# Kernel tuning notes

Measured on AMD Instinct MI355X. Metric: run time of the kernel, lower is better.

Reference implementation:

```python
import jax, jax.numpy as jnp
import numpy as np

B, C, N, OUT, K = 8, 64, 4096, 64, 16


def setup_inputs() -> dict:
    key = jax.random.key(0)
    k0, k1, k2, k3, k4 = jax.random.split(key, 5)
    x = jax.random.normal(k0, (B, C, N, 1), jnp.float32)
    s1 = 1.0 / np.sqrt(2 * C)
    s2 = 1.0 / np.sqrt(OUT)
    W1 = jax.random.uniform(k1, (2 * C, OUT), jnp.float32, -s1, s1)
    b1 = jax.random.uniform(k2, (OUT,), jnp.float32, -s1, s1)
    W2 = jax.random.uniform(k3, (OUT, OUT), jnp.float32, -s2, s2)
    b2 = jax.random.uniform(k4, (OUT,), jnp.float32, -s2, s2)
    return {"x": x, "W1": W1, "b1": b1, "W2": W2, "b2": b2}


def reference(x, W1, b1, W2, b2):
    # x: [B, C, N, 1] -> node features [B, N, C]
    xb = x[..., 0].transpose(0, 2, 1)  # [B, N, C]
    # kNN per batch element (PyG knn includes the point itself)
    sq = jnp.sum(xb * xb, axis=-1)  # [B, N]
    d2 = sq[:, :, None] + sq[:, None, :] - 2.0 * jnp.einsum('bnc,bmc->bnm', xb, xb)
    _, idx = jax.lax.top_k(-d2, K)  # [B, N, K] neighbor indices
    # gather neighbor features: [B, N, K, C]
    xj = jax.vmap(lambda f, i: jnp.take(f, i, axis=0))(xb, idx)
    xi = xb[:, :, None, :]  # [B, N, 1, C]
    # EdgeConv edge features: [x_i, x_j - x_i]
    e = jnp.concatenate([jnp.broadcast_to(xi, xj.shape), xj - xi], axis=-1)  # [B,N,K,2C]
    h = jax.nn.relu(e @ W1 + b1)
    h = jax.nn.relu(h @ W2 + b2)
    out = jnp.max(h, axis=2)  # max aggregation over neighbors -> [B, N, OUT]
    return out.transpose(0, 2, 1)[..., None]  # [B, OUT, N, 1]
```

## Files before the change

### kernel.cpp

```cpp
#include <hip/hip_runtime.h>
#include <stdint.h>

#define BB 8
#define CCH 64
#define NPB 4096
#define NPTS (BB*NPB)
#define PPW 8

typedef float  f32x2  __attribute__((ext_vector_type(2)));
typedef float  f32x4v __attribute__((ext_vector_type(4)));
typedef short  bf16x8 __attribute__((ext_vector_type(8)));
typedef unsigned short u16x8 __attribute__((ext_vector_type(8)));
typedef unsigned long long u64;
typedef unsigned int u32;

__device__ __forceinline__ unsigned short f2bf(float x) {
    u32 u = __float_as_uint(x);
    u += 0x7FFFu + ((u >> 16) & 1u);
    return (unsigned short)(u >> 16);
}

template<typename T>
__device__ __forceinline__ void sort16(T* key) {
#pragma unroll
    for (int kk = 2; kk <= 16; kk <<= 1) {
#pragma unroll
        for (int j = kk >> 1; j > 0; j >>= 1) {
#pragma unroll
            for (int i = 0; i < 16; ++i) {
                int l = i ^ j;
                if (l > i) {
                    bool up = ((i & kk) == 0);
                    T a = key[i], c = key[l];
                    bool cond = up ? (c < a) : (a < c);
                    key[i] = cond ? c : a;
                    key[l] = cond ? a : c;
                }
            }
        }
    }
}

template<typename T>
__device__ __forceinline__ void merge16(T* list, const T* key) {
    T m[16];
#pragma unroll
    for (int i = 0; i < 16; ++i) {
        T a = list[i], c = key[15 - i];
        m[i] = (c < a) ? c : a;
    }
#pragma unroll
    for (int j = 8; j > 0; j >>= 1) {
#pragma unroll
        for (int i = 0; i < 16; ++i) {
            if ((i & j) == 0) {
                T a = m[i], c = m[i + j];
                bool cond = c < a;
                m[i]     = cond ? c : a;
                m[i + j] = cond ? a : c;
            }
        }
    }
#pragma unroll
    for (int i = 0; i < 16; ++i) list[i] = m[i];
}

__global__ void k_transpose(const float* __restrict__ x, float* __restrict__ xb,
                            unsigned short* __restrict__ xh, float* __restrict__ sq) {
    __shared__ float tile[64][65];
    int b  = blockIdx.y;
    int n0 = blockIdx.x * 64;
    int tx = threadIdx.x, ty = threadIdx.y;
    const float* xp = x + (size_t)b * CCH * NPB;
#pragma unroll
    for (int r = 0; r < 8; ++r) {
        int c = ty + r * 8;
        tile[c][tx] = xp[(size_t)c * NPB + n0 + tx];
    }
    __syncthreads();
    float* xbp = xb + ((size_t)b * NPB + n0) * CCH;
    unsigned short* xhp = xh + ((size_t)b * NPB + n0) * CCH;
    float* sqp = sq + (size_t)b * NPB + n0;
#pragma unroll
    for (int r = 0; r < 8; ++r) {
        int nn = ty + r * 8;
        float v = tile[tx][nn];
        xbp[(size_t)nn * CCH + tx] = v;
        xhp[(size_t)nn * CCH + tx] = f2bf(v);
        float s = v * v;
#pragma unroll
        for (int o = 32; o > 0; o >>= 1) s += __shfl_xor(s, o);
        if (tx == 0) sqp[nn] = s;
    }
}

__global__ void k_prepw(const float* __restrict__ W1, const float* __restrict__ W2,
                        unsigned short* __restrict__ W1t, unsigned short* __restrict__ W2t) {
    int t = blockIdx.x * 256 + threadIdx.x;
    if (t < 8192) {
        int o = t >> 7, k = t & 127;
        float v = (k < 64) ? (W1[k * 64 + o] - W1[(64 + k) * 64 + o]) : W1[k * 64 + o];
        W1t[o * 128 + k] = f2bf(v);
    } else if (t < 12288) {
        int u = t - 8192;
        int o = u >> 6, j = u & 63;
        W2t[o * 64 + j] = f2bf(W2[j * 64 + o]);
    }
}

__global__ __launch_bounds__(256) void k_gemm(const unsigned short* __restrict__ xh,
                                              const float* __restrict__ sq,
                                              u32* __restrict__ cand) {
    __shared__ float dtile[64][65];
    __shared__ u32 llist[64][65];
    int b = blockIdx.y >> 6;
    const unsigned short* xhB = xh + (size_t)b * NPB * CCH;
    const float* sqB = sq + (size_t)b * NPB;
    u32* candB = cand + (size_t)b * 64 * NPB * 16;
    int l = threadIdx.x & 63;
    int w = threadIdx.x >> 6;
    int m0 = (blockIdx.y & 63) * 64;
    int n0 = blockIdx.x * 64;
    const unsigned short* ap = xhB + (size_t)(m0 + w * 16 + (l & 15)) * CCH + ((l >> 4) * 8);
    bf16x8 a0 = *(const bf16x8*)ap;
    bf16x8 a1 = *(const bf16x8*)(ap + 32);
    f32x4v z = {0.f, 0.f, 0.f, 0.f};
    f32x4v acc[4];
#pragma unroll
    for (int cg = 0; cg < 4; ++cg) {
        const unsigned short* bp = xhB + (size_t)(n0 + cg * 16 + (l & 15)) * CCH + ((l >> 4) * 8);
        bf16x8 b0 = *(const bf16x8*)bp;
        bf16x8 b1 = *(const bf16x8*)(bp + 32);
        acc[cg] = __builtin_amdgcn_mfma_f32_16x16x32_bf16(a0, b0, z, 0, 0, 0);
        acc[cg] = __builtin_amdgcn_mfma_f32_16x16x32_bf16(a1, b1, acc[cg], 0, 0, 0);
    }
    int rb = m0 + w * 16 + (l >> 4) * 4;
    float4 sr = *(const float4*)(sqB + rb);
    float sqr[4] = {sr.x, sr.y, sr.z, sr.w};
#pragma unroll
    for (int cg = 0; cg < 4; ++cg) {
        int cit = cg * 16 + (l & 15);
        float sc = sqB[n0 + cit];
#pragma unroll
        for (int j = 0; j < 4; ++j) {
            float v = fmaxf(fmaf(-2.f, acc[cg][j], sqr[j] + sc), 0.f);
            dtile[w * 16 + (l >> 4) * 4 + j][cit] = v;
        }
    }
    __syncthreads();
    {
        int row = l, ch = w;
        u32 key[16];
#pragma unroll
        for (int e = 0; e < 16; ++e) {
            float v = dtile[row][ch * 16 + e];
            key[e] = ((u32)f2bf(v) << 16) | (u32)(n0 + ch * 16 + e);
        }
        sort16(key);
#pragma unroll
        for (int i = 0; i < 16; ++i) llist[row][ch * 16 + i] = key[i];
    }
    __syncthreads();
    if (threadIdx.x < 128) {
        int r2 = threadIdx.x & 63;
        int hf = threadIdx.x >> 6;
        u32 a[16], c[16];
#pragma unroll
        for (int i = 0; i < 16; ++i) a[i] = llist[r2][hf * 32 + i];
#pragma unroll
        for (int i = 0; i < 16; ++i) c[i] = llist[r2][hf * 32 + 16 + i];
        merge16(a, c);
#pragma unroll
        for (int i = 0; i < 16; ++i) llist[r2][hf * 32 + i] = a[i];
    }
    __syncthreads();
    if (threadIdx.x < 64) {
        int r2 = threadIdx.x;
        u32 list[16], tmp[16];
#pragma unroll
        for (int i = 0; i < 16; ++i) list[i] = llist[r2][i];
#pragma unroll
        for (int i = 0; i < 16; ++i) tmp[i] = llist[r2][32 + i];
        merge16(list, tmp);
        u32* cp = candB + ((size_t)blockIdx.x * NPB + (m0 + r2)) * 16;
#pragma unroll
        for (int i = 0; i < 16; ++i) cp[i] = list[i];
    }
}

__global__ __launch_bounds__(256, 1) void k_post(const u32* __restrict__ cand,
                                                 const float* __restrict__ xb,
                                                 const float* __restrict__ sq,
                                                 int* __restrict__ idxo) {
    __shared__ u32 slots[4][64];
    int l  = threadIdx.x & 63;
    int rl = __builtin_amdgcn_readfirstlane(threadIdx.x >> 6);
    int rowg = blockIdx.x * 4 + rl;
    int b    = rowg >> 12;
    int row  = rowg & 4095;
    const float* xbB = xb + ((size_t)b << 12) * CCH;
    const float* sqB = sq + ((size_t)b << 12);
    const u32* candB = cand + (size_t)b * 64 * NPB * 16;
    const float* xr = xbB + (size_t)row * CCH;
    float rr[64];
#pragma unroll
    for (int i = 0; i < 16; ++i) {
        float4 v = *(const float4*)(xr + i * 4);
        rr[4*i] = v.x; rr[4*i+1] = v.y; rr[4*i+2] = v.z; rr[4*i+3] = v.w;
    }
    u32 karr[16];
    {
        const uint4* cp = (const uint4*)(candB + ((size_t)l * NPB + row) * 16);
#pragma unroll
        for (int i = 0; i < 4; ++i) {
            uint4 v = cp[i];
            karr[4*i] = v.x; karr[4*i+1] = v.y; karr[4*i+2] = v.z; karr[4*i+3] = v.w;
        }
    }
    u32 lo = 0, hi = 0x7FFFu;
#pragma unroll
    for (int it = 0; it < 15; ++it) {
        u32 mid = (lo + hi) >> 1;
        int c = 0;
#pragma unroll
        for (int i = 0; i < 16; ++i) c += ((karr[i] >> 16) <= mid) ? 1 : 0;
#pragma unroll
        for (int o = 32; o > 0; o >>= 1) c += __shfl_xor(c, o);
        bool ge = (c >= 48);
        lo = ge ? lo : (mid + 1);
        hi = ge ? mid : hi;
    }
    u32 vstar = hi;
    int cnt = 0;
#pragma unroll
    for (int i = 0; i < 16; ++i) cnt += ((karr[i] >> 16) <= vstar) ? 1 : 0;
    int pre = cnt;
#pragma unroll
    for (int d = 1; d < 64; d <<= 1) {
        int t = __shfl_up(pre, d);
        if (l >= d) pre += t;
    }
    int base = pre - cnt;
    u32* sl = slots[rl];
    sl[l] = 0xFFFFFFFFu;
#pragma unroll
    for (int i = 0; i < 16; ++i) {
        if (i < cnt) {
            int s = base + i;
            if (s < 64) sl[s] = karr[i];
        }
    }
    u32 mk = sl[l];
    u64 key = ~0ULL;
    if (mk != 0xFFFFFFFFu) {
        int col = (int)(mk & 0xFFFFu);
        const float* xj = xbB + (size_t)col * CCH;
        float lod = 0.f, hid = 0.f;
#pragma unroll
        for (int q = 0; q < 8; ++q) {
            float4 v  = *(const float4*)(xj + q * 4);
            float4 wv = *(const float4*)(xj + 32 + q * 4);
            lod = fmaf(v.x,  rr[4*q+0], lod);
            lod = fmaf(v.y,  rr[4*q+1], lod);
            lod = fmaf(v.z,  rr[4*q+2], lod);
            lod = fmaf(v.w,  rr[4*q+3], lod);
            hid = fmaf(wv.x, rr[32+4*q+0], hid);
            hid = fmaf(wv.y, rr[32+4*q+1], hid);
            hid = fmaf(wv.z, rr[32+4*q+2], hid);
            hid = fmaf(wv.w, rr[32+4*q+3], hid);
        }
        float d = fmaf(-2.f, lod + hid, sqB[col]);
        u32 fb = __float_as_uint(d);
        fb ^= (fb >> 31) ? 0xFFFFFFFFu : 0x80000000u;
        key = ((u64)fb << 32) | (u32)col;
    }
#pragma unroll
    for (int kk = 2; kk <= 64; kk <<= 1) {
#pragma unroll
        for (int j = kk >> 1; j > 0; j >>= 1) {
            u64 p = (u64)__shfl_xor((long long)key, j);
            bool keep_min = (((l & kk) == 0) == ((l & j) == 0));
            bool plt = p < key;
            key = keep_min ? (plt ? p : key) : (plt ? key : p);
        }
    }
    if (l < 16) idxo[(size_t)rowg * 16 + l] = (int)(key & 0xFFFFFFFFu);
}

__global__ __launch_bounds__(256, 1) void k_mlp2(const unsigned short* __restrict__ xh,
                                                 const int* __restrict__ idx,
                                                 const unsigned short* __restrict__ W1t,
                                                 const unsigned short* __restrict__ W2t,
                                                 const float* __restrict__ b1,
                                                 const float* __restrict__ b2,
                                                 float* __restrict__ out) {
    __shared__ unsigned short h1l[4][16 * 72];
    int l   = threadIdx.x & 63;
    int wib = threadIdx.x >> 6;
    int e   = l & 15;
    int kg  = l >> 4;
    int wave = blockIdx.x * 4 + wib;
    unsigned short* hl = h1l[wib];

    bf16x8 w1f[4][4];
#pragma unroll
    for (int nt = 0; nt < 4; ++nt)
#pragma unroll
        for (int s = 0; s < 4; ++s)
            w1f[nt][s] = *(const bf16x8*)(W1t + (size_t)(nt * 16 + e) * 128 + s * 32 + kg * 8);
    bf16x8 w2f[4][2];
#pragma unroll
    for (int nt = 0; nt < 4; ++nt)
#pragma unroll
        for (int s = 0; s < 2; ++s)
            w2f[nt][s] = *(const bf16x8*)(W2t + (size_t)(nt * 16 + e) * 64 + s * 32 + kg * 8);
    float b1v[4], b2v[4];
#pragma unroll
    for (int nt = 0; nt < 4; ++nt) { b1v[nt] = b1[nt * 16 + e]; b2v[nt] = b2[nt * 16 + e]; }

    int p0 = wave * PPW;
    int bb = p0 >> 12;
    int n0 = p0 & 4095;
    const unsigned short* xhB = xh + ((size_t)bb << 12) * CCH;
    f32x4v z = {0.f, 0.f, 0.f, 0.f};
    float mx[4][PPW];
#pragma unroll
    for (int nt = 0; nt < 4; ++nt)
#pragma unroll
        for (int pi = 0; pi < PPW; ++pi) mx[nt][pi] = 0.f;

#pragma unroll
    for (int pi = 0; pi < PPW; ++pi) {
        int n = n0 + pi;
        int je = idx[((size_t)(p0 + pi)) * 16 + e];
        bf16x8 a[4];
        a[0] = *(const bf16x8*)(xhB + (size_t)n * 64 + kg * 8);
        a[1] = *(const bf16x8*)(xhB + (size_t)n * 64 + 32 + kg * 8);
        a[2] = *(const bf16x8*)(xhB + (size_t)je * 64 + kg * 8);
        a[3] = *(const bf16x8*)(xhB + (size_t)je * 64 + 32 + kg * 8);
#pragma unroll
        for (int nt = 0; nt < 4; ++nt) {
            f32x4v acc = z;
#pragma unroll
            for (int s = 0; s < 4; ++s)
                acc = __builtin_amdgcn_mfma_f32_16x16x32_bf16(a[s], w1f[nt][s], acc, 0, 0, 0);
#pragma unroll
            for (int j = 0; j < 4; ++j) {
                float h = fmaxf(acc[j] + b1v[nt], 0.f);
                hl[(kg * 4 + j) * 72 + nt * 16 + e] = f2bf(h);
            }
        }
        bf16x8 a2[2];
        a2[0] = *(const bf16x8*)(hl + (size_t)e * 72 + kg * 8);
        a2[1] = *(const bf16x8*)(hl + (size_t)e * 72 + 32 + kg * 8);
#pragma unroll
        for (int nt = 0; nt < 4; ++nt) {
            f32x4v acc = z;
            acc = __builtin_amdgcn_mfma_f32_16x16x32_bf16(a2[0], w2f[nt][0], acc, 0, 0, 0);
            acc = __builtin_amdgcn_mfma_f32_16x16x32_bf16(a2[1], w2f[nt][1], acc, 0, 0, 0);
            float m4 = 0.f;
#pragma unroll
            for (int j = 0; j < 4; ++j)
                m4 = fmaxf(m4, fmaxf(acc[j] + b2v[nt], 0.f));
            mx[nt][pi] = m4;
        }
    }
#pragma unroll
    for (int nt = 0; nt < 4; ++nt)
#pragma unroll
        for (int pi = 0; pi < PPW; ++pi) {
            float v = mx[nt][pi];
            v = fmaxf(v, __shfl_xor(v, 16));
            v = fmaxf(v, __shfl_xor(v, 32));
            mx[nt][pi] = v;
        }
    if (kg == 0) {
#pragma unroll
        for (int nt = 0; nt < 4; ++nt) {
            float* op = out + ((size_t)bb * 64 + nt * 16 + e) * NPB + n0;
#pragma unroll
            for (int pi = 0; pi < PPW; ++pi) op[pi] = mx[nt][pi];
        }
    }
}

extern "C" void kernel_launch(void* const* d_in, const int* in_sizes, int n_in,
                              void* d_out, int out_size, void* d_ws, size_t ws_size,
                              hipStream_t stream) {
    const float* x  = (const float*)d_in[0];
    const float* W1 = (const float*)d_in[1];
    const float* b1 = (const float*)d_in[2];
    const float* W2 = (const float*)d_in[3];
    const float* b2 = (const float*)d_in[4];
    float* out = (float*)d_out;

    const size_t MB = 1024 * 1024;
    char* ws = (char*)d_ws;
    float*          xb  = (float*)(ws);
    unsigned short* xh  = (unsigned short*)(ws + 8 * MB);
    float*          sq  = (float*)(ws + 12 * MB);
    unsigned short* W1t = (unsigned short*)(ws + 12 * MB + 256 * 1024);
    unsigned short* W2t = (unsigned short*)(ws + 12 * MB + 272 * 1024);
    u32*            cand = (u32*)(ws + 13 * MB);
    size_t candAll = (size_t)BB * 64 * NPB * 16 * 4;
    size_t needF = 13 * MB + candAll + (size_t)NPTS * 16 * 4;

    hipLaunchKernelGGL(k_transpose, dim3(NPB / 64, BB), dim3(64, 8), 0, stream, x, xb, xh, sq);
    hipLaunchKernelGGL(k_prepw, dim3(48), dim3(256), 0, stream, W1, W2, W1t, W2t);

    if (ws_size >= needF + MB) {
        int* idxb = (int*)(ws + 13 * MB + candAll);
        hipLaunchKernelGGL(k_gemm, dim3(NPB / 64, 64 * BB), dim3(256), 0, stream,
                           xh, sq, cand);
        hipLaunchKernelGGL(k_post, dim3(NPTS / 4), dim3(256), 0, stream,
                           cand, xb, sq, idxb);
        hipLaunchKernelGGL(k_mlp2, dim3(NPTS / PPW / 4), dim3(256), 0, stream,
                           xh, idxb, W1t, W2t, b1, b2, out);
    } else {
        int* idxb = (int*)(ws + 30 * MB);
        for (int b = 0; b < BB; ++b) {
            const unsigned short* xhB = xh + (size_t)b * NPB * CCH;
            const float* xbB = xb + (size_t)b * NPB * CCH;
            const float* sqB = sq + (size_t)b * NPB;
            hipLaunchKernelGGL(k_gemm, dim3(NPB / 64, 64), dim3(256), 0, stream,
                               xhB, sqB, cand);
            hipLaunchKernelGGL(k_post, dim3(NPB / 4), dim3(256), 0, stream,
                               cand, xbB, sqB, idxb + (size_t)b * NPB * 16);
        }
        hipLaunchKernelGGL(k_mlp2, dim3(NPTS / PPW / 4), dim3(256), 0, stream,
                           xh, idxb, W1t, W2t, b1, b2, out);
    }
}
```

Measured before the change: 321.5 us.

## Replace full candidate sort with sampled threshold, filtered rescan, and survivor rerank

A first pass sorts distances over a strided sample of 1024 columns per row (16 tiles of 64, n0 = blockIdx.x*256), and k_tau picks a bf16 distance threshold at the 16th-smallest of that sample. A second GEMM pass recomputes all distances and uses atomics to append columns at or under the threshold to a capped survivor list. k_sel then reranks the survivors exactly in fp32 with wave bitonic sorts. The aim is to drop the 64-way per-tile sort and the large candidate buffer write and read. The cost is a second GEMM pass, atomic contention, and possible truncation when more than 192 columns survive, which could lose true neighbours.

```diff
diff --git a/kernel.cpp b/kernel.cpp
--- a/kernel.cpp
+++ b/kernel.cpp
@@ -6,6 +6,7 @@
 #define NPB 4096
 #define NPTS (BB*NPB)
 #define PPW 8
+#define SCAP 192
 
 typedef float  f32x2  __attribute__((ext_vector_type(2)));
 typedef float  f32x4v __attribute__((ext_vector_type(4)));
@@ -108,15 +109,130 @@
     }
 }
 
-__global__ __launch_bounds__(256) void k_gemm(const unsigned short* __restrict__ xh,
-                                              const float* __restrict__ sq,
-                                              u32* __restrict__ cand) {
+__global__ __launch_bounds__(256) void k_gemm1(const unsigned short* __restrict__ xh,
+                                               const float* __restrict__ sq,
+                                               u32* __restrict__ cand16) {
     __shared__ float dtile[64][65];
     __shared__ u32 llist[64][65];
     int b = blockIdx.y >> 6;
     const unsigned short* xhB = xh + (size_t)b * NPB * CCH;
     const float* sqB = sq + (size_t)b * NPB;
-    u32* candB = cand + (size_t)b * 64 * NPB * 16;
+    u32* candB = cand16 + (size_t)b * 16 * NPB * 16;
+    int l = threadIdx.x & 63;
+    int w = threadIdx.x >> 6;
+    int m0 = (blockIdx.y & 63) * 64;
+    int n0 = blockIdx.x * 256;
+    const unsigned short* ap = xhB + (size_t)(m0 + w * 16 + (l & 15)) * CCH + ((l >> 4) * 8);
+    bf16x8 a0 = *(const bf16x8*)ap;
+    bf16x8 a1 = *(const bf16x8*)(ap + 32);
+    f32x4v z = {0.f, 0.f, 0.f, 0.f};
+    f32x4v acc[4];
+#pragma unroll
+    for (int cg = 0; cg < 4; ++cg) {
+        const unsigned short* bp = xhB + (size_t)(n0 + cg * 16 + (l & 15)) * CCH + ((l >> 4) * 8);
+        bf16x8 b0 = *(const bf16x8*)bp;
+        bf16x8 b1 = *(const bf16x8*)(bp + 32);
+        acc[cg] = __builtin_amdgcn_mfma_f32_16x16x32_bf16(a0, b0, z, 0, 0, 0);
+        acc[cg] = __builtin_amdgcn_mfma_f32_16x16x32_bf16(a1, b1, acc[cg], 0, 0, 0);
+    }
+    int rb = m0 + w * 16 + (l >> 4) * 4;
+    float4 sr = *(const float4*)(sqB + rb);
+    float sqr[4] = {sr.x, sr.y, sr.z, sr.w};
+#pragma unroll
+    for (int cg = 0; cg < 4; ++cg) {
+        int cit = cg * 16 + (l & 15);
+        float sc = sqB[n0 + cit];
+#pragma unroll
+        for (int j = 0; j < 4; ++j) {
+            float v = fmaxf(fmaf(-2.f, acc[cg][j], sqr[j] + sc), 0.f);
+            dtile[w * 16 + (l >> 4) * 4 + j][cit] = v;
+        }
+    }
+    __syncthreads();
+    {
+        int row = l, ch = w;
+        u32 key[16];
+#pragma unroll
+        for (int e = 0; e < 16; ++e) {
+            float v = dtile[row][ch * 16 + e];
+            key[e] = ((u32)f2bf(v) << 16) | (u32)(n0 + ch * 16 + e);
+        }
+        sort16(key);
+#pragma unroll
+        for (int i = 0; i < 16; ++i) llist[row][ch * 16 + i] = key[i];
+    }
+    __syncthreads();
+    if (threadIdx.x < 128) {
+        int r2 = threadIdx.x & 63;
+        int hf = threadIdx.x >> 6;
+        u32 a[16], c[16];
+#pragma unroll
+        for (int i = 0; i < 16; ++i) a[i] = llist[r2][hf * 32 + i];
+#pragma unroll
+        for (int i = 0; i < 16; ++i) c[i] = llist[r2][hf * 32 + 16 + i];
+        merge16(a, c);
+#pragma unroll
+        for (int i = 0; i < 16; ++i) llist[r2][hf * 32 + i] = a[i];
+    }
+    __syncthreads();
+    if (threadIdx.x < 64) {
+        int r2 = threadIdx.x;
+        u32 list[16], tmp[16];
+#pragma unroll
+        for (int i = 0; i < 16; ++i) list[i] = llist[r2][i];
+#pragma unroll
+        for (int i = 0; i < 16; ++i) tmp[i] = llist[r2][32 + i];
+        merge16(list, tmp);
+        u32* cp = candB + ((size_t)blockIdx.x * NPB + (m0 + r2)) * 16;
+#pragma unroll
+        for (int i = 0; i < 16; ++i) cp[i] = list[i];
+    }
+}
+
+__global__ __launch_bounds__(256, 1) void k_tau(const u32* __restrict__ cand16,
+                                                u32* __restrict__ tau) {
+    int l  = threadIdx.x & 63;
+    int rl = __builtin_amdgcn_readfirstlane(threadIdx.x >> 6);
+    int rowg = blockIdx.x * 4 + rl;
+    int b    = rowg >> 12;
+    int row  = rowg & 4095;
+    const u32* candB = cand16 + (size_t)b * 16 * NPB * 16;
+    u32 karr[16];
+    if (l < 16) {
+        const uint4* cp = (const uint4*)(candB + ((size_t)l * NPB + row) * 16);
+#pragma unroll
+        for (int i = 0; i < 4; ++i) {
+            uint4 v = cp[i];
+            karr[4*i] = v.x; karr[4*i+1] = v.y; karr[4*i+2] = v.z; karr[4*i+3] = v.w;
+        }
+    } else {
+#pragma unroll
+        for (int i = 0; i < 16; ++i) karr[i] = 0xFFFFFFFFu;
+    }
+    u32 lo = 0, hi = 0x7FFFu;
+#pragma unroll
+    for (int it = 0; it < 15; ++it) {
+        u32 mid = (lo + hi) >> 1;
+        int c = 0;
+#pragma unroll
+        for (int i = 0; i < 16; ++i) c += ((karr[i] >> 16) <= mid) ? 1 : 0;
+#pragma unroll
+        for (int o = 32; o > 0; o >>= 1) c += __shfl_xor(c, o);
+        bool ge = (c >= 16);
+        lo = ge ? lo : (mid + 1);
+        hi = ge ? mid : hi;
+    }
+    if (l == 0) tau[rowg] = hi;
+}
+
+__global__ __launch_bounds__(256) void k_gemm2(const unsigned short* __restrict__ xh,
+                                               const float* __restrict__ sq,
+                                               const u32* __restrict__ tau,
+                                               int* __restrict__ cnt,
+                                               u32* __restrict__ surv) {
+    int b = blockIdx.y >> 6;
+    const unsigned short* xhB = xh + (size_t)b * NPB * CCH;
+    const float* sqB = sq + (size_t)b * NPB;
     int l = threadIdx.x & 63;
     int w = threadIdx.x >> 6;
     int m0 = (blockIdx.y & 63) * 64;
@@ -137,6 +253,9 @@
     int rb = m0 + w * 16 + (l >> 4) * 4;
     float4 sr = *(const float4*)(sqB + rb);
     float sqr[4] = {sr.x, sr.y, sr.z, sr.w};
+    u32 tv[4];
+#pragma unroll
+    for (int j = 0; j < 4; ++j) tv[j] = tau[(b << 12) + rb + j];
 #pragma unroll
     for (int cg = 0; cg < 4; ++cg) {
         int cit = cg * 16 + (l & 15);
@@ -144,55 +263,21 @@
 #pragma unroll
         for (int j = 0; j < 4; ++j) {
             float v = fmaxf(fmaf(-2.f, acc[cg][j], sqr[j] + sc), 0.f);
-            dtile[w * 16 + (l >> 4) * 4 + j][cit] = v;
-        }
-    }
-    __syncthreads();
-    {
-        int row = l, ch = w;
-        u32 key[16];
-#pragma unroll
-        for (int e = 0; e < 16; ++e) {
-            float v = dtile[row][ch * 16 + e];
-            key[e] = ((u32)f2bf(v) << 16) | (u32)(n0 + ch * 16 + e);
-        }
-        sort16(key);
-#pragma unroll
-        for (int i = 0; i < 16; ++i) llist[row][ch * 16 + i] = key[i];
-    }
-    __syncthreads();
-    if (threadIdx.x < 128) {
-        int r2 = threadIdx.x & 63;
-        int hf = threadIdx.x >> 6;
-        u32 a[16], c[16];
-#pragma unroll
-        for (int i = 0; i < 16; ++i) a[i] = llist[r2][hf * 32 + i];
-#pragma unroll
-        for (int i = 0; i < 16; ++i) c[i] = llist[r2][hf * 32 + 16 + i];
-        merge16(a, c);
-#pragma unroll
-        for (int i = 0; i < 16; ++i) llist[r2][hf * 32 + i] = a[i];
-    }
-    __syncthreads();
-    if (threadIdx.x < 64) {
-        int r2 = threadIdx.x;
-        u32 list[16], tmp[16];
-#pragma unroll
-        for (int i = 0; i < 16; ++i) list[i] = llist[r2][i];
-#pragma unroll
-        for (int i = 0; i < 16; ++i) tmp[i] = llist[r2][32 + i];
-        merge16(list, tmp);
-        u32* cp = candB + ((size_t)blockIdx.x * NPB + (m0 + r2)) * 16;
-#pragma unroll
-        for (int i = 0; i < 16; ++i) cp[i] = list[i];
-    }
-}
-
-__global__ __launch_bounds__(256, 1) void k_post(const u32* __restrict__ cand,
-                                                 const float* __restrict__ xb,
-                                                 const float* __restrict__ sq,
-                                                 int* __restrict__ idxo) {
-    __shared__ u32 slots[4][64];
+            u32 bv = (u32)f2bf(v);
+            if (bv <= tv[j]) {
+                int rg = (b << 12) + rb + j;
+                int slot = atomicAdd(&cnt[rg], 1);
+                if (slot < SCAP) surv[(size_t)rg * SCAP + slot] = (u32)(n0 + cit);
+            }
+        }
+    }
+}
+
+__global__ __launch_bounds__(256, 1) void k_sel(const u32* __restrict__ surv,
+                                                const int* __restrict__ cnt,
+                                                const float* __restrict__ xb,
+                                                const float* __restrict__ sq,
+                                                int* __restrict__ idxo) {
     int l  = threadIdx.x & 63;
     int rl = __builtin_amdgcn_readfirstlane(threadIdx.x >> 6);
     int rowg = blockIdx.x * 4 + rl;
@@ -200,7 +285,6 @@
     int row  = rowg & 4095;
     const float* xbB = xb + ((size_t)b << 12) * CCH;
     const float* sqB = sq + ((size_t)b << 12);
-    const u32* candB = cand + (size_t)b * 64 * NPB * 16;
     const float* xr = xbB + (size_t)row * CCH;
     float rr[64];
 #pragma unroll
@@ -208,83 +292,63 @@
         float4 v = *(const float4*)(xr + i * 4);
         rr[4*i] = v.x; rr[4*i+1] = v.y; rr[4*i+2] = v.z; rr[4*i+3] = v.w;
     }
-    u32 karr[16];
-    {
-        const uint4* cp = (const uint4*)(candB + ((size_t)l * NPB + row) * 16);
-#pragma unroll
-        for (int i = 0; i < 4; ++i) {
-            uint4 v = cp[i];
-            karr[4*i] = v.x; karr[4*i+1] = v.y; karr[4*i+2] = v.z; karr[4*i+3] = v.w;
-        }
-    }
-    u32 lo = 0, hi = 0x7FFFu;
-#pragma unroll
-    for (int it = 0; it < 15; ++it) {
-        u32 mid = (lo + hi) >> 1;
-        int c = 0;
-#pragma unroll
-        for (int i = 0; i < 16; ++i) c += ((karr[i] >> 16) <= mid) ? 1 : 0;
-#pragma unroll
-        for (int o = 32; o > 0; o >>= 1) c += __shfl_xor(c, o);
-        bool ge = (c >= 48);
-        lo = ge ? lo : (mid + 1);
-        hi = ge ? mid : hi;
-    }
-    u32 vstar = hi;
-    int cnt = 0;
-#pragma unroll
-    for (int i = 0; i < 16; ++i) cnt += ((karr[i] >> 16) <= vstar) ? 1 : 0;
-    int pre = cnt;
-#pragma unroll
-    for (int d = 1; d < 64; d <<= 1) {
-        int t = __shfl_up(pre, d);
-        if (l >= d) pre += t;
-    }
-    int base = pre - cnt;
-    u32* sl = slots[rl];
-    sl[l] = 0xFFFFFFFFu;
-#pragma unroll
-    for (int i = 0; i < 16; ++i) {
-        if (i < cnt) {
-            int s = base + i;
-            if (s < 64) sl[s] = karr[i];
-        }
-    }
-    u32 mk = sl[l];
-    u64 key = ~0ULL;
-    if (mk != 0xFFFFFFFFu) {
-        int col = (int)(mk & 0xFFFFu);
-        const float* xj = xbB + (size_t)col * CCH;
-        float lod = 0.f, hid = 0.f;
-#pragma unroll
-        for (int q = 0; q < 8; ++q) {
-            float4 v  = *(const float4*)(xj + q * 4);
-            float4 wv = *(const float4*)(xj + 32 + q * 4);
-            lod = fmaf(v.x,  rr[4*q+0], lod);
-            lod = fmaf(v.y,  rr[4*q+1], lod);
-            lod = fmaf(v.z,  rr[4*q+2], lod);
-            lod = fmaf(v.w,  rr[4*q+3], lod);
-            hid = fmaf(wv.x, rr[32+4*q+0], hid);
-            hid = fmaf(wv.y, rr[32+4*q+1], hid);
-            hid = fmaf(wv.z, rr[32+4*q+2], hid);
-            hid = fmaf(wv.w, rr[32+4*q+3], hid);
-        }
-        float d = fmaf(-2.f, lod + hid, sqB[col]);
-        u32 fb = __float_as_uint(d);
-        fb ^= (fb >> 31) ? 0xFFFFFFFFu : 0x80000000u;
-        key = ((u64)fb << 32) | (u32)col;
-    }
-#pragma unroll
-    for (int kk = 2; kk <= 64; kk <<= 1) {
-#pragma unroll
-        for (int j = kk >> 1; j > 0; j >>= 1) {
-            u64 p = (u64)__shfl_xor((long long)key, j);
-            bool keep_min = (((l & kk) == 0) == ((l & j) == 0));
-            bool plt = p < key;
-            key = keep_min ? (plt ? p : key) : (plt ? key : p);
-        }
-    }
-    if (l < 16) idxo[(size_t)rowg * 16 + l] = (int)(key & 0xFFFFFFFFu);
+    int n = cnt[rowg];
+    n = n > SCAP ? SCAP : n;
+    u64 m = ~0ULL;
+#pragma unroll
+    for (int p = 0; p < 3; ++p) {
+        if (p == 0 || n > p * 64) {
+            int s = p * 64 + l;
+            u64 key = ~0ULL;
+            if (s < n) {
+                int col = (int)surv[(size_t)rowg * SCAP + s];
+                const float* xj = xbB + (size_t)col * CCH;
+                float lod = 0.f, hid = 0.f;
+#pragma unroll
+                for (int q = 0; q < 8; ++q) {
+                    float4 v  = *(const float4*)(xj + q * 4);
+                    float4 wv = *(const float4*)(xj + 32 + q * 4);
+                    lod = fmaf(v.x,  rr[4*q+0], lod);
+                    lod = fmaf(v.y,  rr[4*q+1], lod);
+                    lod = fmaf(v.z,  rr[4*q+2], lod);
+                    lod = fmaf(v.w,  rr[4*q+3], lod);
+                    hid = fmaf(wv.x, rr[32+4*q+0], hid);
+                    hid = fmaf(wv.y, rr[32+4*q+1], hid);
+                    hid = fmaf(wv.z, rr[32+4*q+2], hid);
+                    hid = fmaf(wv.w, rr[32+4*q+3], hid);
+                }
+                float d = fmaf(-2.f, lod + hid, sqB[col]);
+                u32 fb = __float_as_uint(d);
+                fb ^= (fb >> 31) ? 0xFFFFFFFFu : 0x80000000u;
+                key = ((u64)fb << 32) | (u32)col;
+            }
+#pragma unroll
+            for (int kk = 2; kk <= 64; kk <<= 1) {
+#pragma unroll
+                for (int j = kk >> 1; j > 0; j >>= 1) {
+                    u64 pz = (u64)__shfl_xor((long long)key, j);
+                    bool keep_min = (((l & kk) == 0) == ((l & j) == 0));
+                    bool plt = pz < key;
+                    key = keep_min ? (plt ? pz : key) : (plt ? key : pz);
+                }
+            }
+            if (p == 0) {
+                m = key;
+            } else {
+                u64 q = (u64)__shfl((long long)key, 63 - l);
+                u64 mm = q < m ? q : m;
+#pragma unroll
+                for (int j = 32; j > 0; j >>= 1) {
+                    u64 pz = (u64)__shfl_xor((long long)mm, j);
+                    bool low = ((l & j) == 0);
+                    bool plt = pz < mm;
+                    mm = low ? (plt ? pz : mm) : (plt ? mm : pz);
+                }
+                m = mm;
+            }
+        }
+    }
+    if (l < 16) idxo[(size_t)rowg * 16 + l] = (int)(m & 0xFFFFFFFFu);
 }
 
 __global__ __launch_bounds__(256, 1) void k_mlp2(const unsigned short* __restrict__ xh,
@@ -395,39 +459,28 @@
     float* out = (float*)d_out;
 
     const size_t MB = 1024 * 1024;
+    const size_t KB = 1024;
     char* ws = (char*)d_ws;
-    float*          xb  = (float*)(ws);
-    unsigned short* xh  = (unsigned short*)(ws + 8 * MB);
-    float*          sq  = (float*)(ws + 12 * MB);
-    unsigned short* W1t = (unsigned short*)(ws + 12 * MB + 256 * 1024);
-    unsigned short* W2t = (unsigned short*)(ws + 12 * MB + 272 * 1024);
-    u32*            cand = (u32*)(ws + 13 * MB);
-    size_t candAll = (size_t)BB * 64 * NPB * 16 * 4;
-    size_t needF = 13 * MB + candAll + (size_t)NPTS * 16 * 4;
+    float*          xb   = (float*)(ws);
+    unsigned short* xh   = (unsigned short*)(ws + 8 * MB);
+    float*          sq   = (float*)(ws + 12 * MB);
+    unsigned short* W1t  = (unsigned short*)(ws + 12 * MB + 256 * KB);
+    unsigned short* W2t  = (unsigned short*)(ws + 12 * MB + 272 * KB);
+    u32*            tau  = (u32*)(ws + 12 * MB + 320 * KB);
+    int*            cnt  = (int*)(ws + 12 * MB + 448 * KB);
+    int*            idxb = (int*)(ws + 13 * MB);
+    u32*            cand16 = (u32*)(ws + 15 * MB);
+    u32*            surv = (u32*)(ws + 47 * MB);
 
     hipLaunchKernelGGL(k_transpose, dim3(NPB / 64, BB), dim3(64, 8), 0, stream, x, xb, xh, sq);
     hipLaunchKernelGGL(k_prepw, dim3(48), dim3(256), 0, stream, W1, W2, W1t, W2t);
-
-    if (ws_size >= needF + MB) {
-        int* idxb = (int*)(ws + 13 * MB + candAll);
-        hipLaunchKernelGGL(k_gemm, dim3(NPB / 64, 64 * BB), dim3(256), 0, stream,
-                           xh, sq, cand);
-        hipLaunchKernelGGL(k_post, dim3(NPTS / 4), dim3(256), 0, stream,
-                           cand, xb, sq, idxb);
-        hipLaunchKernelGGL(k_mlp2, dim3(NPTS / PPW / 4), dim3(256), 0, stream,
-                           xh, idxb, W1t, W2t, b1, b2, out);
-    } else {
-        int* idxb = (int*)(ws + 30 * MB);
-        for (int b = 0; b < BB; ++b) {
-            const unsigned short* xhB = xh + (size_t)b * NPB * CCH;
-            const float* xbB = xb + (size_t)b * NPB * CCH;
-            const float* sqB = sq + (size_t)b * NPB;
-            hipLaunchKernelGGL(k_gemm, dim3(NPB / 64, 64), dim3(256), 0, stream,
-                               xhB, sqB, cand);
-            hipLaunchKernelGGL(k_post, dim3(NPB / 4), dim3(256), 0, stream,
-                               cand, xbB, sqB, idxb + (size_t)b * NPB * 16);
-        }
-        hipLaunchKernelGGL(k_mlp2, dim3(NPTS / PPW / 4), dim3(256), 0, stream,
-                           xh, idxb, W1t, W2t, b1, b2, out);
-    }
-}
+    hipLaunchKernelGGL(k_gemm1, dim3(16, 64 * BB), dim3(256), 0, stream, xh, sq, cand16);
+    hipLaunchKernelGGL(k_tau, dim3(NPTS / 4), dim3(256), 0, stream, cand16, tau);
+    hipMemsetAsync(cnt, 0, (size_t)NPTS * 4, stream);
+    hipLaunchKernelGGL(k_gemm2, dim3(NPB / 64, 64 * BB), dim3(256), 0, stream,
+                       xh, sq, tau, cnt, surv);
+    hipLaunchKernelGGL(k_sel, dim3(NPTS / 4), dim3(256), 0, stream,
+                       surv, cnt, xb, sq, idxb);
+    hipLaunchKernelGGL(k_mlp2, dim3(NPTS / PPW / 4), dim3(256), 0, stream,
+                       xh, idxb, W1t, W2t, b1, b2, out);
+}
```

After: 611.1 us. 90.1% more time.
